# Kernel tuning notes

Hardware: AMD Instinct MI355X
Metric: run time of the kernel (lower is better)

## Reference

```python
import jax, jax.numpy as jnp
import numpy as np

D_MODEL, N_LEVELS, N_HEADS, N_POINTS = 256, 4, 8, 4
SHAPES = [(100, 100), (50, 50), (25, 25), (13, 13)]  # (H, W) per level


def setup_inputs() -> dict:
    key = jax.random.key(0)
    ks = jax.random.split(key, 8)
    N = 2
    C = D_MODEL
    Len_in = sum(h * w for h, w in SHAPES)
    Lq = Len_in  # encoder self-attention
    query = jax.random.normal(ks[0], (N, Lq, C), jnp.float32)
    reference_points = jax.random.uniform(ks[1], (N, Lq, N_LEVELS, 2), dtype=jnp.float32)
    input_flatten = jax.random.normal(ks[2], (N, Len_in, C), jnp.float32)
    input_spatial_shapes = np.array(SHAPES, dtype=np.int64)
    areas = input_spatial_shapes[:, 0] * input_spatial_shapes[:, 1]
    input_level_start_index = np.concatenate([[0], np.cumsum(areas)[:-1]]).astype(np.int64)
    s = 1.0 / np.sqrt(C)
    Wv = jax.random.uniform(ks[3], (C, C), jnp.float32, -s, s)
    bv = jnp.zeros((C,), jnp.float32)
    # sampling_offsets: small random weight + the module's grid bias init
    Woff = jax.random.normal(ks[4], (N_HEADS * N_LEVELS * N_POINTS * 2, C), jnp.float32) * 0.01
    thetas = jnp.arange(N_HEADS, dtype=jnp.float32) * (2.0 * np.pi / N_HEADS)
    grid = jnp.stack([jnp.cos(thetas), jnp.sin(thetas)], -1)  # (M,2)
    grid = grid / jnp.max(jnp.abs(grid), axis=-1, keepdims=True)
    grid = jnp.tile(grid[:, None, None, :], (1, N_LEVELS, N_POINTS, 1))
    grid = grid * (jnp.arange(N_POINTS, dtype=jnp.float32) + 1.0)[None, None, :, None]
    boff = grid.reshape(-1)
    Wa = jax.random.normal(ks[5], (N_HEADS * N_LEVELS * N_POINTS, C), jnp.float32) * 0.02
    ba = jnp.zeros((N_HEADS * N_LEVELS * N_POINTS,), jnp.float32)
    Wo = jax.random.uniform(ks[6], (C, C), jnp.float32, -s, s)
    bo = jnp.zeros((C,), jnp.float32)
    return {
        'query': query, 'reference_points': reference_points, 'input_flatten': input_flatten,
        'input_spatial_shapes': input_spatial_shapes, 'input_level_start_index': input_level_start_index,
        'Wv': Wv, 'bv': bv, 'Woff': Woff, 'boff': boff, 'Wa': Wa, 'ba': ba, 'Wo': Wo, 'bo': bo,
    }


def _msda_forward(query, reference_points, input_flatten, shapes, starts,
                  Wv, bv, Woff, boff, Wa, ba, Wo, bo):
    N, Lq, C = query.shape
    M, L, P = N_HEADS, N_LEVELS, N_POINTS
    D = C // M
    value = (input_flatten @ Wv.T + bv).reshape(N, -1, M, D)  # (N, Len_in, M, D)
    off = (query @ Woff.T + boff).reshape(N, Lq, M, L, P, 2)
    attn = jax.nn.softmax((query @ Wa.T + ba).reshape(N, Lq, M, L * P), axis=-1)
    attn = attn.reshape(N, Lq, M, L, P)
    # offset_normalizer = (W_l, H_l)
    norm = jnp.asarray(shapes[:, ::-1].copy(), jnp.float32)  # (L, 2)
    loc = reference_points[:, :, None, :, None, :] + off / norm[None, None, None, :, None, :]
    grids = 2.0 * loc - 1.0  # (N, Lq, M, L, P, 2), grid_sample convention
    out = jnp.zeros((N, Lq, M, D), query.dtype)
    for l in range(L):
        H, W = int(shapes[l, 0]), int(shapes[l, 1])
        s0 = int(starts[l])
        v = value[:, s0:s0 + H * W]  # (N, H*W, M, D)
        # align_corners=False unnormalization
        gx = ((grids[:, :, :, l, :, 0] + 1.0) * W - 1.0) / 2.0  # (N, Lq, M, P)
        gy = ((grids[:, :, :, l, :, 1] + 1.0) * H - 1.0) / 2.0
        x0 = jnp.floor(gx); y0 = jnp.floor(gy)
        fx = gx - x0;       fy = gy - y0
        x0i = x0.astype(jnp.int32); y0i = y0.astype(jnp.int32)

        def gather(iy, ix):
            valid = (iy >= 0) & (iy < H) & (ix >= 0) & (ix < W)
            lin = jnp.clip(iy, 0, H - 1) * W + jnp.clip(ix, 0, W - 1)  # (N, Lq, M, P)
            lin2 = lin.transpose(0, 1, 3, 2).reshape(N, Lq * P, M)
            g = jnp.take_along_axis(v, lin2[..., None], axis=1)  # (N, Lq*P, M, D)
            g = g.reshape(N, Lq, P, M, D).transpose(0, 1, 3, 2, 4)  # (N, Lq, M, P, D)
            return g * valid[..., None]  # zero padding outside

        s00 = gather(y0i, x0i)
        s01 = gather(y0i, x0i + 1)
        s10 = gather(y0i + 1, x0i)
        s11 = gather(y0i + 1, x0i + 1)
        sampled = (s00 * ((1 - fy) * (1 - fx))[..., None] + s01 * ((1 - fy) * fx)[..., None]
                   + s10 * (fy * (1 - fx))[..., None] + s11 * (fy * fx)[..., None])
        out = out + jnp.einsum('nqmp,nqmpd->nqmd', attn[:, :, :, l], sampled)
    out = out.reshape(N, Lq, C)
    return out @ Wo.T + bo


def reference(query, reference_points, input_flatten, input_spatial_shapes, input_level_start_index,
              Wv, bv, Woff, boff, Wa, ba, Wo, bo):
    shapes = np.asarray(input_spatial_shapes)
    starts = np.asarray(input_level_start_index)
    return _msda_forward(query, reference_points, input_flatten, shapes, starts,
                         Wv, bv, Woff, boff, Wa, ba, Wo, bo)
```

## Files before the change

### kernel.cpp

```cpp
#include <hip/hip_runtime.h>
#include <math.h>

#define NB   2
#define LQ   13294
#define NROWS (NB*LQ)
#define CDIM 256

typedef unsigned short u16;
typedef unsigned int   u32;
typedef short bf16x8 __attribute__((ext_vector_type(8)));
typedef float f32x4  __attribute__((ext_vector_type(4)));

struct alignas(8) U16x4 { u16 x, y, z, w; };

__device__ __forceinline__ u16 f2bf(float f) {
    u32 u = __builtin_bit_cast(u32, f);
    u += 0x7FFFu + ((u >> 16) & 1u);
    return (u16)(u >> 16);
}
__device__ __forceinline__ float bf2f(u16 h) {
    u32 u = ((u32)h) << 16;
    return __builtin_bit_cast(float, u);
}

__global__ __launch_bounds__(256)
void prep_all(const float4* __restrict__ query, const float4* __restrict__ inflat,
              const float* __restrict__ Wv, const float* __restrict__ Woff,
              const float* __restrict__ Wa, const float* __restrict__ Wo,
              const float* __restrict__ boff, const float* __restrict__ ba,
              u16* __restrict__ qb, u16* __restrict__ ib,
              u16* __restrict__ wb, float* __restrict__ biascat) {
    const int b = blockIdx.x;
    const int t = threadIdx.x;
    if (b < 6647) {
        int i = b * 256 + t;
        float4 v = query[i];
        U16x4 o{f2bf(v.x), f2bf(v.y), f2bf(v.z), f2bf(v.w)};
        *(U16x4*)&qb[(size_t)i * 4] = o;
    } else if (b < 13294) {
        int i = (b - 6647) * 256 + t;
        float4 v = inflat[i];
        U16x4 o{f2bf(v.x), f2bf(v.y), f2bf(v.z), f2bf(v.w)};
        *(U16x4*)&ib[(size_t)i * 4] = o;
    } else {
        int i = (b - 13294) * 256 + t;
        float v;
        if      (i <  65536) v = Wv[i];
        else if (i < 131072) v = Woff[i - 65536];
        else if (i < 163840) v = Wa[i - 131072];
        else                 v = Wo[i - 163840];
        wb[i] = f2bf(v);
        if (b == 13294) {
            biascat[t] = boff[t];
            if (t < 128) biascat[256 + t] = ba[t];
        }
    }
}

__device__ __forceinline__ void gemm_core64(
    const u16* __restrict__ A, const u16* __restrict__ Bw, int M, int row0,
    u16* As, u16* Bs, f32x4 (&acc)[2][2]) {
    const int tid  = threadIdx.x;
    const int wave = tid >> 6;
    const int lane = tid & 63;
    const int ln16 = lane & 15;
    const int kq   = lane >> 4;
    const int wrow = (wave >> 1) * 32;
    const int wcol = (wave & 1) * 32;

    #pragma unroll
    for (int kt = 0; kt < 4; ++kt) {
        const int k0 = kt * 64;
        #pragma unroll
        for (int it = 0; it < 2; ++it) {
            int chunk = it * 256 + tid;
            int row = chunk >> 3;
            int ch  = chunk & 7;
            int gra = min(row0 + row, M - 1);
            float4 va = *(const float4*)(A  + (size_t)gra * 256 + k0 + ch * 8);
            float4 vb = *(const float4*)(Bw + (size_t)row * 256 + k0 + ch * 8);
            *(float4*)&As[row * 64 + (ch ^ (row & 7)) * 8] = va;
            *(float4*)&Bs[row * 64 + (ch ^ (row & 7)) * 8] = vb;
        }
        __syncthreads();
        #pragma unroll
        for (int kf = 0; kf < 2; ++kf) {
            int ck = kf * 4 + kq;
            bf16x8 a[2], b[2];
            #pragma unroll
            for (int i = 0; i < 2; ++i) {
                int r = wrow + i * 16 + ln16;
                a[i] = *(const bf16x8*)&As[r * 64 + ((ck ^ (r & 7)) * 8)];
                int c = wcol + i * 16 + ln16;
                b[i] = *(const bf16x8*)&Bs[c * 64 + ((ck ^ (c & 7)) * 8)];
            }
            #pragma unroll
            for (int i = 0; i < 2; ++i)
                #pragma unroll
                for (int j = 0; j < 2; ++j)
                    acc[i][j] = __builtin_amdgcn_mfma_f32_16x16x32_bf16(
                        a[i], b[j], acc[i][j], 0, 0, 0);
        }
        __syncthreads();
    }
}

__global__ __launch_bounds__(256, 4)
void gemm_front(const u16* __restrict__ qb, const u16* __restrict__ ib,
                const u16* __restrict__ wb, const float* __restrict__ bv,
                const float* __restrict__ bcat, u16* __restrict__ value,
                float* __restrict__ offb, float* __restrict__ logit, int M) {
    __shared__ u16 As[64 * 64];
    __shared__ u16 Bs[64 * 64];
    const int s    = blockIdx.x;
    const int row0 = blockIdx.y * 64;
    const u16* A  = (s < 4) ? ib : qb;
    const u16* Bw = (s < 4) ? wb + (size_t)s * 64 * 256
                            : wb + 65536 + (size_t)(s - 4) * 64 * 256;
    const float* bias = (s < 4) ? bv + s * 64 : bcat + (s - 4) * 64;

    f32x4 acc[2][2] = {};
    gemm_core64(A, Bw, M, row0, As, Bs, acc);

    const int lane = threadIdx.x & 63;
    const int wave = threadIdx.x >> 6;
    const int ln16 = lane & 15, kq = lane >> 4;
    const int wrow = (wave >> 1) * 32, wcol = (wave & 1) * 32;
    #pragma unroll
    for (int j = 0; j < 2; ++j) {
        int lc = wcol + j * 16 + ln16;
        float bj = bias[lc];
        #pragma unroll
        for (int i = 0; i < 2; ++i) {
            #pragma unroll
            for (int r = 0; r < 4; ++r) {
                int gr = row0 + wrow + i * 16 + kq * 4 + r;
                if (gr < M) {
                    float o = acc[i][j][r] + bj;
                    if (s < 4)
                        value[(size_t)gr * 256 + s * 64 + lc] = f2bf(o);
                    else {
                        int gc = (s - 4) * 64 + lc;
                        if (gc < 256) offb[(size_t)gr * 256 + gc] = o;
                        else          logit[(size_t)gr * 128 + (gc - 256)] = o;
                    }
                }
            }
        }
    }
}

__global__ __launch_bounds__(256, 4)
void gemm_out(const u16* __restrict__ A, const u16* __restrict__ Bw0,
              const float* __restrict__ bias, float* __restrict__ C, int M) {
    __shared__ u16 As[64 * 64];
    __shared__ u16 Bs[64 * 64];
    const int s    = blockIdx.x;
    const int row0 = blockIdx.y * 64;
    const u16* Bw = Bw0 + (size_t)s * 64 * 256;

    f32x4 acc[2][2] = {};
    gemm_core64(A, Bw, M, row0, As, Bs, acc);

    const int lane = threadIdx.x & 63;
    const int wave = threadIdx.x >> 6;
    const int ln16 = lane & 15, kq = lane >> 4;
    const int wrow = (wave >> 1) * 32, wcol = (wave & 1) * 32;
    #pragma unroll
    for (int j = 0; j < 2; ++j) {
        int gc = s * 64 + wcol + j * 16 + ln16;
        float bj = bias[gc];
        #pragma unroll
        for (int i = 0; i < 2; ++i) {
            #pragma unroll
            for (int r = 0; r < 4; ++r) {
                int gr = row0 + wrow + i * 16 + kq * 4 + r;
                if (gr < M) C[(size_t)gr * 256 + gc] = acc[i][j][r] + bj;
            }
        }
    }
}

__global__ __launch_bounds__(256)
void msda_sample(const u16* __restrict__ value,
                 const float* __restrict__ refpts,
                 const float* __restrict__ off,
                 const float* __restrict__ logits,
                 u16* __restrict__ tmp) {
    __shared__ float sAw[4][8][16];
    __shared__ int   sLin[4][8][17][4];
    __shared__ float sW[4][8][17][4];

    const int t  = threadIdx.x;
    const int qb = blockIdx.x * 4;

    if (t < 32) {
        const int qi = t >> 3, m = t & 7;
        const float* lg = logits + (size_t)(qb + qi) * 128 + m * 16;
        float e[16];
        float mx = -1e30f;
        #pragma unroll
        for (int i = 0; i < 16; ++i) { e[i] = lg[i]; mx = fmaxf(mx, e[i]); }
        float s = 0.f;
        #pragma unroll
        for (int i = 0; i < 16; ++i) { e[i] = __expf(e[i] - mx); s += e[i]; }
        const float inv = 1.f / s;
        #pragma unroll
        for (int i = 0; i < 16; ++i) sAw[qi][m][i] = e[i] * inv;
    }
    __syncthreads();

    #pragma unroll
    for (int j2 = 0; j2 < 2; ++j2) {
        const int job = t + j2 * 256;
        const int qi = job >> 7;
        const int m  = (job >> 4) & 7;
        const int p  = job & 15;
        const int l  = p >> 2, pp = p & 3;
        const int q  = qb + qi;
        const int n  = (q >= LQ) ? 1 : 0;

        const int W = (l == 0) ? 100 : (l == 1) ? 50 : (l == 2) ? 25 : 13;
        const int H = W;
        const int st = (l == 0) ? 0 : (l == 1) ? 10000 : (l == 2) ? 12500 : 13125;

        const float rx = refpts[(size_t)q * 8 + l * 2 + 0];
        const float ry = refpts[(size_t)q * 8 + l * 2 + 1];
        const float ox = off[(size_t)q * 256 + m * 32 + (l * 4 + pp) * 2 + 0];
        const float oy = off[(size_t)q * 256 + m * 32 + (l * 4 + pp) * 2 + 1];

        const float locx = rx + ox / (float)W;
        const float locy = ry + oy / (float)H;
        const float grx = 2.f * locx - 1.f;
        const float gry = 2.f * locy - 1.f;
        const float gx = ((grx + 1.f) * (float)W - 1.f) * 0.5f;
        const float gy = ((gry + 1.f) * (float)H - 1.f) * 0.5f;
        const float x0f = floorf(gx), y0f = floorf(gy);
        const float fx = gx - x0f, fy = gy - y0f;
        const int x0 = (int)x0f, y0 = (int)y0f;
        const int x1 = x0 + 1, y1 = y0 + 1;

        const int cx0 = min(max(x0, 0), W - 1);
        const int cx1 = min(max(x1, 0), W - 1);
        const int cy0 = min(max(y0, 0), H - 1);
        const int cy1 = min(max(y1, 0), H - 1);
        const bool vx0 = (x0 >= 0) & (x0 < W);
        const bool vx1 = (x1 >= 0) & (x1 < W);
        const bool vy0 = (y0 >= 0) & (y0 < H);
        const bool vy1 = (y1 >= 0) & (y1 < H);

        const float aw = sAw[qi][m][p];
        const int base = n * LQ + st;
        sLin[qi][m][p][0] = base + cy0 * W + cx0;
        sLin[qi][m][p][1] = base + cy0 * W + cx1;
        sLin[qi][m][p][2] = base + cy1 * W + cx0;
        sLin[qi][m][p][3] = base + cy1 * W + cx1;
        sW[qi][m][p][0] = (vy0 & vx0) ? aw * (1.f - fy) * (1.f - fx) : 0.f;
        sW[qi][m][p][1] = (vy0 & vx1) ? aw * (1.f - fy) * fx         : 0.f;
        sW[qi][m][p][2] = (vy1 & vx0) ? aw * fy * (1.f - fx)         : 0.f;
        sW[qi][m][p][3] = (vy1 & vx1) ? aw * fy * fx                 : 0.f;
    }
    __syncthreads();

    const int qi = t >> 6;
    const int m  = (t >> 3) & 7;
    const int e  = t & 7;
    const int q  = qb + qi;
    const u16* vch = value + m * 32 + e * 4;

    float ax = 0.f, ay = 0.f, az = 0.f, aw_ = 0.f;
    #pragma unroll
    for (int g = 0; g < 4; ++g) {
        U16x4 raw[16];
        float4 Wt4[4];
        #pragma unroll
        for (int pp = 0; pp < 4; ++pp) {
            int p = g * 4 + pp;
            int4 L = *(const int4*)&sLin[qi][m][p][0];
            Wt4[pp] = *(const float4*)&sW[qi][m][p][0];
            raw[pp * 4 + 0] = *(const U16x4*)(vch + (size_t)L.x * 256);
            raw[pp * 4 + 1] = *(const U16x4*)(vch + (size_t)L.y * 256);
            raw[pp * 4 + 2] = *(const U16x4*)(vch + (size_t)L.z * 256);
            raw[pp * 4 + 3] = *(const U16x4*)(vch + (size_t)L.w * 256);
        }
        #pragma unroll
        for (int pp = 0; pp < 4; ++pp) {
            const float* wp = (const float*)&Wt4[pp];
            #pragma unroll
            for (int c = 0; c < 4; ++c) {
                U16x4 r = raw[pp * 4 + c];
                float wgt = wp[c];
                ax  += wgt * bf2f(r.x);
                ay  += wgt * bf2f(r.y);
                az  += wgt * bf2f(r.z);
                aw_ += wgt * bf2f(r.w);
            }
        }
    }
    U16x4 o{f2bf(ax), f2bf(ay), f2bf(az), f2bf(aw_)};
    *(U16x4*)&tmp[(size_t)q * 256 + m * 32 + e * 4] = o;
}

extern "C" void kernel_launch(void* const* d_in, const int* in_sizes, int n_in,
                              void* d_out, int out_size, void* d_ws, size_t ws_size,
                              hipStream_t stream) {
    const float* query  = (const float*)d_in[0];
    const float* refpts = (const float*)d_in[1];
    const float* inflat = (const float*)d_in[2];
    const float* Wv   = (const float*)d_in[5];
    const float* bv   = (const float*)d_in[6];
    const float* Woff = (const float*)d_in[7];
    const float* boff = (const float*)d_in[8];
    const float* Wa   = (const float*)d_in[9];
    const float* ba   = (const float*)d_in[10];
    const float* Wo   = (const float*)d_in[11];
    const float* bo   = (const float*)d_in[12];
    float* out = (float*)d_out;

    char* ws = (char*)d_ws;
    constexpr size_t SZ16 = (size_t)NROWS * 256 * 2;
    constexpr size_t SZ32 = (size_t)NROWS * 256 * 4;
    constexpr size_t SZL  = (size_t)NROWS * 128 * 4;
    u16*   qb    = (u16*)(ws);
    u16*   ib    = (u16*)(ws + SZ16);
    u16*   value = (u16*)(ws + 2 * SZ16);
    float* offb  = (float*)(ws + 3 * SZ16);
    float* logit = (float*)(ws + 3 * SZ16 + SZ32);
    u16*   wb    = (u16*)(ws + 3 * SZ16 + SZ32 + SZL);
    float* bcat  = (float*)(ws + 3 * SZ16 + SZ32 + SZL + 229376 * 2);
    u16*   tmp   = qb;

    const int RG = (NROWS + 63) / 64;

    hipLaunchKernelGGL(prep_all, dim3(14190), dim3(256), 0, stream,
                       (const float4*)query, (const float4*)inflat,
                       Wv, Woff, Wa, Wo, boff, ba, qb, ib, wb, bcat);

    gemm_front<<<dim3(10, RG), dim3(256), 0, stream>>>(
        qb, ib, wb, bv, bcat, value, offb, logit, NROWS);

    hipLaunchKernelGGL(msda_sample, dim3(NROWS / 4), dim3(256), 0, stream,
                       value, refpts, offb, logit, tmp);

    gemm_out<<<dim3(4, RG), dim3(256), 0, stream>>>(
        tmp, wb + 163840, bo, out, NROWS);
}
```

Baseline: 229.8 us.

## Use 128x128 GEMM tiles with direct global-to-LDS loads

Both GEMM kernels move from 64x64 to 128x128 output tiles, so each wave computes a 4x4 grid of MFMA fragments. This gives more operand reuse per LDS load and halves the grid in both dimensions. Tile loads now use global_load_lds to write straight into shared memory, with the XOR swizzle moved to the global source address so the LDS read pattern stays the same. In exchange the kernels use more registers and LDS (occupancy hint drops to 3) and launch fewer blocks, which may underfill the GPU.

```diff
diff --git a/kernel.cpp b/kernel.cpp
--- a/kernel.cpp
+++ b/kernel.cpp
@@ -21,6 +21,12 @@
 __device__ __forceinline__ float bf2f(u16 h) {
     u32 u = ((u32)h) << 16;
     return __builtin_bit_cast(float, u);
+}
+
+__device__ __forceinline__ void gload_lds16(const void* g, void* l) {
+    __builtin_amdgcn_global_load_lds(
+        (__attribute__((address_space(1))) void*)g,
+        (__attribute__((address_space(3))) void*)l, 16, 0, 0);
 }
 
 __global__ __launch_bounds__(256)
@@ -57,47 +63,46 @@
     }
 }
 
-__device__ __forceinline__ void gemm_core64(
+__device__ __forceinline__ void gemm_core128(
     const u16* __restrict__ A, const u16* __restrict__ Bw, int M, int row0,
-    u16* As, u16* Bs, f32x4 (&acc)[2][2]) {
+    u16* As, u16* Bs, f32x4 (&acc)[4][4]) {
     const int tid  = threadIdx.x;
+    const int lane = tid & 63;
     const int wave = tid >> 6;
-    const int lane = tid & 63;
     const int ln16 = lane & 15;
     const int kq   = lane >> 4;
-    const int wrow = (wave >> 1) * 32;
-    const int wcol = (wave & 1) * 32;
+    const int wr   = (wave >> 1) * 64;
+    const int wc   = (wave & 1) * 64;
 
     #pragma unroll
     for (int kt = 0; kt < 4; ++kt) {
         const int k0 = kt * 64;
         #pragma unroll
-        for (int it = 0; it < 2; ++it) {
+        for (int it = 0; it < 4; ++it) {
             int chunk = it * 256 + tid;
             int row = chunk >> 3;
             int ch  = chunk & 7;
+            int chs = (ch ^ (row & 7)) * 8;
             int gra = min(row0 + row, M - 1);
-            float4 va = *(const float4*)(A  + (size_t)gra * 256 + k0 + ch * 8);
-            float4 vb = *(const float4*)(Bw + (size_t)row * 256 + k0 + ch * 8);
-            *(float4*)&As[row * 64 + (ch ^ (row & 7)) * 8] = va;
-            *(float4*)&Bs[row * 64 + (ch ^ (row & 7)) * 8] = vb;
+            gload_lds16(A  + (size_t)gra * 256 + k0 + chs, As + chunk * 8);
+            gload_lds16(Bw + (size_t)row * 256 + k0 + chs, Bs + chunk * 8);
         }
         __syncthreads();
         #pragma unroll
         for (int kf = 0; kf < 2; ++kf) {
-            int ck = kf * 4 + kq;
-            bf16x8 a[2], b[2];
-            #pragma unroll
-            for (int i = 0; i < 2; ++i) {
-                int r = wrow + i * 16 + ln16;
+            const int ck = kf * 4 + kq;
+            bf16x8 a[4], b[4];
+            #pragma unroll
+            for (int i = 0; i < 4; ++i) {
+                int r = wr + i * 16 + ln16;
                 a[i] = *(const bf16x8*)&As[r * 64 + ((ck ^ (r & 7)) * 8)];
-                int c = wcol + i * 16 + ln16;
+                int c = wc + i * 16 + ln16;
                 b[i] = *(const bf16x8*)&Bs[c * 64 + ((ck ^ (c & 7)) * 8)];
             }
             #pragma unroll
-            for (int i = 0; i < 2; ++i)
+            for (int i = 0; i < 4; ++i)
                 #pragma unroll
-                for (int j = 0; j < 2; ++j)
+                for (int j = 0; j < 4; ++j)
                     acc[i][j] = __builtin_amdgcn_mfma_f32_16x16x32_bf16(
                         a[i], b[j], acc[i][j], 0, 0, 0);
         }
@@ -105,76 +110,74 @@
     }
 }
 
-__global__ __launch_bounds__(256, 4)
+__global__ __launch_bounds__(256, 3)
 void gemm_front(const u16* __restrict__ qb, const u16* __restrict__ ib,
                 const u16* __restrict__ wb, const float* __restrict__ bv,
                 const float* __restrict__ bcat, u16* __restrict__ value,
                 float* __restrict__ offb, float* __restrict__ logit, int M) {
-    __shared__ u16 As[64 * 64];
-    __shared__ u16 Bs[64 * 64];
+    __shared__ u16 As[128 * 64];
+    __shared__ u16 Bs[128 * 64];
     const int s    = blockIdx.x;
-    const int row0 = blockIdx.y * 64;
-    const u16* A  = (s < 4) ? ib : qb;
-    const u16* Bw = (s < 4) ? wb + (size_t)s * 64 * 256
-                            : wb + 65536 + (size_t)(s - 4) * 64 * 256;
-    const float* bias = (s < 4) ? bv + s * 64 : bcat + (s - 4) * 64;
-
-    f32x4 acc[2][2] = {};
-    gemm_core64(A, Bw, M, row0, As, Bs, acc);
+    const int row0 = blockIdx.y * 128;
+    const u16* A  = (s < 2) ? ib : qb;
+    const u16* Bw = wb + (size_t)s * 32768;
+    const float* bias = (s < 2) ? bv + s * 128 : bcat + (s - 2) * 128;
+
+    f32x4 acc[4][4] = {};
+    gemm_core128(A, Bw, M, row0, As, Bs, acc);
 
     const int lane = threadIdx.x & 63;
     const int wave = threadIdx.x >> 6;
     const int ln16 = lane & 15, kq = lane >> 4;
-    const int wrow = (wave >> 1) * 32, wcol = (wave & 1) * 32;
-    #pragma unroll
-    for (int j = 0; j < 2; ++j) {
-        int lc = wcol + j * 16 + ln16;
+    const int wr = (wave >> 1) * 64, wc = (wave & 1) * 64;
+    #pragma unroll
+    for (int j = 0; j < 4; ++j) {
+        int lc = wc + j * 16 + ln16;
         float bj = bias[lc];
         #pragma unroll
-        for (int i = 0; i < 2; ++i) {
+        for (int i = 0; i < 4; ++i) {
             #pragma unroll
             for (int r = 0; r < 4; ++r) {
-                int gr = row0 + wrow + i * 16 + kq * 4 + r;
+                int gr = row0 + wr + i * 16 + kq * 4 + r;
                 if (gr < M) {
                     float o = acc[i][j][r] + bj;
-                    if (s < 4)
-                        value[(size_t)gr * 256 + s * 64 + lc] = f2bf(o);
-                    else {
-                        int gc = (s - 4) * 64 + lc;
-                        if (gc < 256) offb[(size_t)gr * 256 + gc] = o;
-                        else          logit[(size_t)gr * 128 + (gc - 256)] = o;
-                    }
+                    if (s < 2)
+                        value[(size_t)gr * 256 + s * 128 + lc] = f2bf(o);
+                    else if (s < 4)
+                        offb[(size_t)gr * 256 + (s - 2) * 128 + lc] = o;
+                    else
+                        logit[(size_t)gr * 128 + lc] = o;
                 }
             }
         }
     }
 }
 
-__global__ __launch_bounds__(256, 4)
+__global__ __launch_bounds__(256, 3)
 void gemm_out(const u16* __restrict__ A, const u16* __restrict__ Bw0,
               const float* __restrict__ bias, float* __restrict__ C, int M) {
-    __shared__ u16 As[64 * 64];
-    __shared__ u16 Bs[64 * 64];
+    __shared__ u16 As[128 * 64];
+    __shared__ u16 Bs[128 * 64];
     const int s    = blockIdx.x;
-    const int row0 = blockIdx.y * 64;
-    const u16* Bw = Bw0 + (size_t)s * 64 * 256;
-
-    f32x4 acc[2][2] = {};
-    gemm_core64(A, Bw, M, row0, As, Bs, acc);
+    const int row0 = blockIdx.y * 128;
+    const u16* Bw = Bw0 + (size_t)s * 32768;
+
+    f32x4 acc[4][4] = {};
+    gemm_core128(A, Bw, M, row0, As, Bs, acc);
 
     const int lane = threadIdx.x & 63;
     const int wave = threadIdx.x >> 6;
     const int ln16 = lane & 15, kq = lane >> 4;
-    const int wrow = (wave >> 1) * 32, wcol = (wave & 1) * 32;
-    #pragma unroll
-    for (int j = 0; j < 2; ++j) {
-        int gc = s * 64 + wcol + j * 16 + ln16;
+    const int wr = (wave >> 1) * 64, wc = (wave & 1) * 64;
+    #pragma unroll
+    for (int j = 0; j < 4; ++j) {
+        int gc = s * 128 + wc + j * 16 + ln16;
         float bj = bias[gc];
         #pragma unroll
-        for (int i = 0; i < 2; ++i) {
+        for (int i = 0; i < 4; ++i) {
             #pragma unroll
             for (int r = 0; r < 4; ++r) {
-                int gr = row0 + wrow + i * 16 + kq * 4 + r;
+                int gr = row0 + wr + i * 16 + kq * 4 + r;
                 if (gr < M) C[(size_t)gr * 256 + gc] = acc[i][j][r] + bj;
             }
         }
@@ -330,18 +333,18 @@
     float* bcat  = (float*)(ws + 3 * SZ16 + SZ32 + SZL + 229376 * 2);
     u16*   tmp   = qb;
 
-    const int RG = (NROWS + 63) / 64;
+    const int RG = (NROWS + 127) / 128;
 
     hipLaunchKernelGGL(prep_all, dim3(14190), dim3(256), 0, stream,
                        (const float4*)query, (const float4*)inflat,
                        Wv, Woff, Wa, Wo, boff, ba, qb, ib, wb, bcat);
 
-    gemm_front<<<dim3(10, RG), dim3(256), 0, stream>>>(
+    gemm_front<<<dim3(5, RG), dim3(256), 0, stream>>>(
         qb, ib, wb, bv, bcat, value, offb, logit, NROWS);
 
     hipLaunchKernelGGL(msda_sample, dim3(NROWS / 4), dim3(256), 0, stream,
                        value, refpts, offb, logit, tmp);
 
-    gemm_out<<<dim3(4, RG), dim3(256), 0, stream>>>(
+    gemm_out<<<dim3(2, RG), dim3(256), 0, stream>>>(
         tmp, wb + 163840, bo, out, NROWS);
 }
```

Measured after the change: 232.5 us. No clear change (+1.2%).
